# Optimization experiments

Hardware: AMD Instinct MI355X
Metric: run time of the kernel (lower is better)

Reference implementation:

```python
import jax, jax.numpy as jnp
import numpy as np

NUM_CLASSES = 2
TIME_STEPS = 1000
B = 16
L = 1024


def _cosine_schedule(num_steps, s=0.01):
    # Faithful port of beta_schedule(..., 'cosine') + __init__ log buffers (float64 -> float32).
    t = np.arange(0, num_steps + 1, dtype=np.float64)
    f_t = np.cos((t / num_steps + s) / (1 + s) * np.pi * 0.5) ** 2
    alpha_bars = f_t / f_t[0]
    alphas = np.clip(alpha_bars[1:] / alpha_bars[:-1], 0.001, 0.999)
    alphas = np.sqrt(alphas)
    log_alphas = np.log(alphas)
    log_alpha_bars = np.cumsum(log_alphas)
    log_1_minus_alphas = np.log(1.0 - np.exp(log_alphas) + 1e-40)
    log_1_minus_alpha_bars = np.log(1.0 - np.exp(log_alpha_bars) + 1e-40)
    f32 = lambda x: jnp.asarray(x, jnp.float32)
    return f32(log_alphas), f32(log_1_minus_alphas), f32(log_alpha_bars), f32(log_1_minus_alpha_bars)


def setup_inputs() -> dict:
    key = jax.random.key(0)
    k1, k2, k3 = jax.random.split(key, 3)
    # log_x_t: log one-hot, as produced by log_sample_categorical (clamp min 1e-30 -> log)
    x_t = jax.random.randint(k1, (B, 1, L, L), 0, NUM_CLASSES)
    onehot = jax.nn.one_hot(x_t, NUM_CLASSES, axis=1, dtype=jnp.float32)  # (B,K,1,L,L)
    log_x_t = jnp.log(jnp.clip(onehot, 1e-30))
    # log_x_0: log-softmax distribution, as produced by predict_x_0 (F.log_softmax over class dim)
    logits0 = jax.random.normal(k2, (B, NUM_CLASSES, 1, L, L), jnp.float32)
    log_x_0 = jax.nn.log_softmax(logits0, axis=1)
    la, l1a, lab, l1ab = _cosine_schedule(TIME_STEPS)
    t = jax.random.randint(k3, (B,), 0, TIME_STEPS).astype(jnp.int64)
    return {
        'log_x_t': log_x_t,
        'log_x_0': log_x_0,
        'log_alphas': la,
        'log_1_minus_alphas': l1a,
        'log_alpha_bars': lab,
        'log_1_minus_alpha_bars': l1ab,
        't': t,
    }


def reference(log_x_t, log_x_0, log_alphas, log_1_minus_alphas, log_alpha_bars, log_1_minus_alpha_bars, t):
    # MultinomialDiffusion.q_posterior: gather(extract) + log_add_exp + where-mask + logsumexp over class dim.
    K = log_x_0.shape[1]
    log_K = jnp.log(jnp.asarray(K, log_x_0.dtype))
    ext = lambda a, tt: a[tt].reshape(-1, 1, 1, 1, 1)  # extract(a, t, x_shape)

    # q_pred(log_x_0, t-1) with t-1 clamped to 0
    t_m1 = jnp.maximum(t - 1, 0)
    log_EV_qxtmin_x0 = jnp.logaddexp(
        log_x_0 + ext(log_alpha_bars, t_m1),
        ext(log_1_minus_alpha_bars, t_m1) - log_K,
    )
    # where t == 0, posterior mean is log_x_0 itself
    t_b = t.reshape(-1, 1, 1, 1, 1)
    log_EV_qxtmin_x0 = jnp.where(t_b == 0, log_x_0, log_EV_qxtmin_x0)

    # q_pred_one_step(log_x_t, t)
    log_one_step = jnp.logaddexp(
        log_x_t + ext(log_alphas, t),
        ext(log_1_minus_alphas, t) - log_K,
    )

    unnormed = log_EV_qxtmin_x0 + log_one_step
    return unnormed - jax.nn.logsumexp(unnormed, axis=1, keepdims=True)
```

## Files before the change

### kernel.cpp

```cpp
#include <hip/hip_runtime.h>


#define LL (1024 * 1024)
#define BLOCKS_PER_B 256
#define ITER 4

typedef float vfloat4 __attribute__((ext_vector_type(4)));

__global__ __launch_bounds__(256) void qposterior_kernel(
    const float* __restrict__ lxt,
    const float* __restrict__ lx0,
    const float* __restrict__ la,
    const float* __restrict__ l1a,
    const float* __restrict__ lab,
    const float* __restrict__ l1ab,
    const int* __restrict__ tarr,
    float* __restrict__ out)
{
    const float LOGK = 0.6931471805599453f;

    int bid   = blockIdx.x;
    int b     = bid >> 8;
    int local = bid & (BLOCKS_PER_B - 1);

    int tb = tarr[b];
    bool t0 = (tb == 0);
    float C = la[tb];
    float D = l1a[tb] - LOGK;
    float mm = fmaxf(C, D);
    float s_hot = mm + __logf(1.0f + __expf(fminf(C, D) - mm));
    float delta = s_hot - D;

    float a = 0.f, c = 0.f, apc = 0.f;
    if (!t0) {
        int tm1 = tb - 1;
        a   = __expf(lab[tm1]);
        c   = 0.5f * __expf(l1ab[tm1]);
        apc = a + c;
    }

    const float* xt_p  = lxt + b * (2 * LL);
    const float* x0_p  = lx0 + b * (2 * LL);
    float*       out_p = out + b * (2 * LL);

    int gbase = local * (ITER * 256) + threadIdx.x;

    if (!t0) {
        vfloat4 xt[ITER], x0[ITER];
#pragma unroll
        for (int it = 0; it < ITER; ++it) {
            int e = (gbase + it * 256) * 4;
            xt[it] = *reinterpret_cast<const vfloat4*>(xt_p + e);
            x0[it] = *reinterpret_cast<const vfloat4*>(x0_p + e);
        }
        __builtin_amdgcn_sched_barrier(0);

#pragma unroll
        for (int it = 0; it < ITER; ++it) {
            int e = (gbase + it * 256) * 4;
            vfloat4 r0, r1;
#pragma unroll
            for (int i = 0; i < 4; ++i) {
                float l00 = x0[it][i];
                float p  = __expf(l00);
                float e0 = __logf(fmaf(a, p, c));
                float e1 = __logf(fmaf(-a, p, apc));
                float d  = e0 - e1;
                float sd    = (xt[it][i] > -35.0f) ? delta : -delta;
                float Delta = d + sd;
                float m  = fmaxf(-Delta, 0.0f);
                float o0 = -(m + __logf(1.0f + __expf(-fabsf(Delta))));
                r0[i] = o0;
                r1[i] = o0 - Delta;
            }
            *reinterpret_cast<vfloat4*>(out_p + e)      = r0;
            *reinterpret_cast<vfloat4*>(out_p + e + LL) = r1;
        }
    } else {
#pragma unroll
        for (int it = 0; it < ITER; ++it) {
            int e = (gbase + it * 256) * 4;
            vfloat4 xt = *reinterpret_cast<const vfloat4*>(xt_p + e);
            vfloat4 x0 = *reinterpret_cast<const vfloat4*>(x0_p + e);
            vfloat4 x1 = *reinterpret_cast<const vfloat4*>(x0_p + e + LL);
            vfloat4 r0, r1;
#pragma unroll
            for (int i = 0; i < 4; ++i) {
                float d = x0[i] - x1[i];
                float sd    = (xt[i] > -35.0f) ? delta : -delta;
                float Delta = d + sd;
                float m  = fmaxf(-Delta, 0.0f);
                float o0 = -(m + __logf(1.0f + __expf(-fabsf(Delta))));
                r0[i] = o0;
                r1[i] = o0 - Delta;
            }
            *reinterpret_cast<vfloat4*>(out_p + e)      = r0;
            *reinterpret_cast<vfloat4*>(out_p + e + LL) = r1;
        }
    }
}

extern "C" void kernel_launch(void* const* d_in, const int* in_sizes, int n_in,
                              void* d_out, int out_size, void* d_ws, size_t ws_size,
                              hipStream_t stream) {
    const float* lxt  = (const float*)d_in[0];
    const float* lx0  = (const float*)d_in[1];
    const float* la   = (const float*)d_in[2];
    const float* l1a  = (const float*)d_in[3];
    const float* lab  = (const float*)d_in[4];
    const float* l1ab = (const float*)d_in[5];
    const int*   tarr = (const int*)d_in[6];
    float*       out  = (float*)d_out;

    const int grid  = 16 * BLOCKS_PER_B;
    const int block = 256;

    qposterior_kernel<<<grid, block, 0, stream>>>(lxt, lx0, la, l1a, lab, l1ab, tarr, out);
}
```

Before: 288.8 us.

## Double-buffer input tiles through LDS with async global_load_lds pipelining

Reduces the grid to fewer persistent-style blocks that each process eight tiles. Inputs for the non-zero-t path are staged into double-buffered LDS via asynchronous global-to-LDS loads, with manual vmcnt waits so the next tile's loads overlap the current tile's compute and stores. This aims to keep more memory traffic in flight per wave. In exchange it lowers occupancy and relies on hand-counted waitcnt values that also include outstanding stores.

```diff
diff --git a/kernel.cpp b/kernel.cpp
--- a/kernel.cpp
+++ b/kernel.cpp
@@ -2,10 +2,14 @@
 
 
 #define LL (1024 * 1024)
-#define BLOCKS_PER_B 256
-#define ITER 4
+#define BLOCKS_PER_B 64
+#define TILES 8
+#define TILE_E 2048
+#define GRID (16 * BLOCKS_PER_B)
 
 typedef float vfloat4 __attribute__((ext_vector_type(4)));
+typedef const __attribute__((address_space(1))) void cgv_t;
+typedef __attribute__((address_space(3))) void lsv_t;
 
 __global__ __launch_bounds__(256) void qposterior_kernel(
     const float* __restrict__ lxt,
@@ -17,23 +21,29 @@
     const int* __restrict__ tarr,
     float* __restrict__ out)
 {
+    __shared__ float lds_xt[2][TILE_E];
+    __shared__ float lds_x0[2][TILE_E];
+
     const float LOGK = 0.6931471805599453f;
 
     int bid   = blockIdx.x;
-    int b     = bid >> 8;
+    int b     = bid >> 6;
     int local = bid & (BLOCKS_PER_B - 1);
+    int tid   = threadIdx.x;
+    int w     = tid >> 6;
+    int lane  = tid & 63;
 
-    int tb = tarr[b];
-    bool t0 = (tb == 0);
-    float C = la[tb];
-    float D = l1a[tb] - LOGK;
+    int tb_ = tarr[b];
+    bool t0 = (tb_ == 0);
+    float C = la[tb_];
+    float D = l1a[tb_] - LOGK;
     float mm = fmaxf(C, D);
     float s_hot = mm + __logf(1.0f + __expf(fminf(C, D) - mm));
     float delta = s_hot - D;
 
     float a = 0.f, c = 0.f, apc = 0.f;
     if (!t0) {
-        int tm1 = tb - 1;
+        int tm1 = tb_ - 1;
         a   = __expf(lab[tm1]);
         c   = 0.5f * __expf(l1ab[tm1]);
         apc = a + c;
@@ -43,59 +53,88 @@
     const float* x0_p  = lx0 + b * (2 * LL);
     float*       out_p = out + b * (2 * LL);
 
-    int gbase = local * (ITER * 256) + threadIdx.x;
+    int blk_base = local * (TILES * TILE_E);
+    int wbase    = w * 512;
 
     if (!t0) {
-        vfloat4 xt[ITER], x0[ITER];
+        auto stage = [&](int buf, int t) {
+            int gb = blk_base + t * TILE_E + wbase + lane * 4;
+            __builtin_amdgcn_global_load_lds((cgv_t*)(xt_p + gb),
+                                             (lsv_t*)&lds_xt[buf][wbase],       16, 0, 0);
+            __builtin_amdgcn_global_load_lds((cgv_t*)(xt_p + gb + 256),
+                                             (lsv_t*)&lds_xt[buf][wbase + 256], 16, 0, 0);
+            __builtin_amdgcn_global_load_lds((cgv_t*)(x0_p + gb),
+                                             (lsv_t*)&lds_x0[buf][wbase],       16, 0, 0);
+            __builtin_amdgcn_global_load_lds((cgv_t*)(x0_p + gb + 256),
+                                             (lsv_t*)&lds_x0[buf][wbase + 256], 16, 0, 0);
+        };
+
+        auto compute_store = [&](int buf, int t) {
+            int gb = blk_base + t * TILE_E + wbase + lane * 4;
+            vfloat4 r0[2], r1[2];
 #pragma unroll
-        for (int it = 0; it < ITER; ++it) {
-            int e = (gbase + it * 256) * 4;
-            xt[it] = *reinterpret_cast<const vfloat4*>(xt_p + e);
-            x0[it] = *reinterpret_cast<const vfloat4*>(x0_p + e);
-        }
+            for (int i = 0; i < 2; ++i) {
+                vfloat4 xt4 = *(vfloat4*)&lds_xt[buf][wbase + i * 256 + lane * 4];
+                vfloat4 x04 = *(vfloat4*)&lds_x0[buf][wbase + i * 256 + lane * 4];
+#pragma unroll
+                for (int j = 0; j < 4; ++j) {
+                    float p  = __expf(x04[j]);
+                    float e0 = __logf(fmaf(a, p, c));
+                    float e1 = __logf(fmaf(-a, p, apc));
+                    float d  = e0 - e1;
+                    float sd    = (xt4[j] > -35.0f) ? delta : -delta;
+                    float Delta = d + sd;
+                    float m  = fmaxf(-Delta, 0.0f);
+                    float o0 = -(m + __logf(1.0f + __expf(-fabsf(Delta))));
+                    r0[i][j] = o0;
+                    r1[i][j] = o0 - Delta;
+                }
+            }
+            *(vfloat4*)(out_p + gb)            = r0[0];
+            *(vfloat4*)(out_p + gb + 256)      = r0[1];
+            *(vfloat4*)(out_p + gb + LL)       = r1[0];
+            *(vfloat4*)(out_p + gb + LL + 256) = r1[1];
+        };
+
+        stage(0, 0);
+        stage(1, 1);
+        asm volatile("s_waitcnt vmcnt(4)" ::: "memory");
         __builtin_amdgcn_sched_barrier(0);
+        compute_store(0, 0);
 
 #pragma unroll
-        for (int it = 0; it < ITER; ++it) {
-            int e = (gbase + it * 256) * 4;
-            vfloat4 r0, r1;
+        for (int t = 1; t < TILES - 1; ++t) {
+            stage((t + 1) & 1, t + 1);
+            asm volatile("s_waitcnt vmcnt(8)" ::: "memory");
+            __builtin_amdgcn_sched_barrier(0);
+            compute_store(t & 1, t);
+        }
+
+        asm volatile("s_waitcnt vmcnt(4)" ::: "memory");
+        __builtin_amdgcn_sched_barrier(0);
+        compute_store((TILES - 1) & 1, TILES - 1);
+    } else {
+        for (int t = 0; t < TILES; ++t) {
 #pragma unroll
-            for (int i = 0; i < 4; ++i) {
-                float l00 = x0[it][i];
-                float p  = __expf(l00);
-                float e0 = __logf(fmaf(a, p, c));
-                float e1 = __logf(fmaf(-a, p, apc));
-                float d  = e0 - e1;
-                float sd    = (xt[it][i] > -35.0f) ? delta : -delta;
-                float Delta = d + sd;
-                float m  = fmaxf(-Delta, 0.0f);
-                float o0 = -(m + __logf(1.0f + __expf(-fabsf(Delta))));
-                r0[i] = o0;
-                r1[i] = o0 - Delta;
+            for (int j = 0; j < 2; ++j) {
+                int e = blk_base + t * TILE_E + (j * 256 + tid) * 4;
+                vfloat4 xt = *(const vfloat4*)(xt_p + e);
+                vfloat4 x0 = *(const vfloat4*)(x0_p + e);
+                vfloat4 x1 = *(const vfloat4*)(x0_p + e + LL);
+                vfloat4 r0, r1;
+#pragma unroll
+                for (int i = 0; i < 4; ++i) {
+                    float d = x0[i] - x1[i];
+                    float sd    = (xt[i] > -35.0f) ? delta : -delta;
+                    float Delta = d + sd;
+                    float m  = fmaxf(-Delta, 0.0f);
+                    float o0 = -(m + __logf(1.0f + __expf(-fabsf(Delta))));
+                    r0[i] = o0;
+                    r1[i] = o0 - Delta;
+                }
+                *(vfloat4*)(out_p + e)      = r0;
+                *(vfloat4*)(out_p + e + LL) = r1;
             }
-            *reinterpret_cast<vfloat4*>(out_p + e)      = r0;
-            *reinterpret_cast<vfloat4*>(out_p + e + LL) = r1;
-        }
-    } else {
-#pragma unroll
-        for (int it = 0; it < ITER; ++it) {
-            int e = (gbase + it * 256) * 4;
-            vfloat4 xt = *reinterpret_cast<const vfloat4*>(xt_p + e);
-            vfloat4 x0 = *reinterpret_cast<const vfloat4*>(x0_p + e);
-            vfloat4 x1 = *reinterpret_cast<const vfloat4*>(x0_p + e + LL);
-            vfloat4 r0, r1;
-#pragma unroll
-            for (int i = 0; i < 4; ++i) {
-                float d = x0[i] - x1[i];
-                float sd    = (xt[i] > -35.0f) ? delta : -delta;
-                float Delta = d + sd;
-                float m  = fmaxf(-Delta, 0.0f);
-                float o0 = -(m + __logf(1.0f + __expf(-fabsf(Delta))));
-                r0[i] = o0;
-                r1[i] = o0 - Delta;
-            }
-            *reinterpret_cast<vfloat4*>(out_p + e)      = r0;
-            *reinterpret_cast<vfloat4*>(out_p + e + LL) = r1;
         }
     }
 }
@@ -112,8 +151,5 @@
     const int*   tarr = (const int*)d_in[6];
     float*       out  = (float*)d_out;
 
-    const int grid  = 16 * BLOCKS_PER_B;
-    const int block = 256;
-
-    qposterior_kernel<<<grid, block, 0, stream>>>(lxt, lx0, la, l1a, lab, l1ab, tarr, out);
+    qposterior_kernel<<<GRID, 256, 0, stream>>>(lxt, lx0, la, l1a, lab, l1ab, tarr, out);
 }
```

Result: slower. 300.3 us (+4.0%).
